# Optimization experiments

Measured on AMD Instinct MI355X. Metric: run time of the kernel, lower is better.

The kernel has to match this reference:

```python
import jax, jax.numpy as jnp
import numpy as np


def _maxpool2x2(x):
    # x: [B, C, H, W] -> [B, C, H//2, W//2]
    B, C, H, W = x.shape
    return x.reshape(B, C, H // 2, 2, W // 2, 2).max(axis=(3, 5))


def setup_inputs() -> dict:
    key = jax.random.key(0)
    ks = jax.random.split(key, 6)
    B, CH, H, W = 16, 128, 64, 64
    W_SCALE = 0.05  # keep pre-softmax logits in a sane range
    x = jax.random.normal(ks[0], (B, CH, H, W), dtype=jnp.float32)
    w_theta = jax.random.normal(ks[1], (CH // 8, CH), dtype=jnp.float32) * W_SCALE
    w_phi = jax.random.normal(ks[2], (CH // 8, CH), dtype=jnp.float32) * W_SCALE
    w_g = jax.random.normal(ks[3], (CH // 2, CH), dtype=jnp.float32) * W_SCALE
    w_o = jax.random.normal(ks[4], (CH, CH // 2), dtype=jnp.float32) * W_SCALE
    gamma = jax.random.normal(ks[5], (1,), dtype=jnp.float32)  # torch inits to 0; randomized for non-trivial output
    return {"x": x, "w_theta": w_theta, "w_phi": w_phi, "w_g": w_g, "w_o": w_o, "gamma": gamma}


def reference(x, w_theta, w_phi, w_g, w_o, gamma):
    B, C, H, W = x.shape
    N = H * W
    # 1x1 convs are channel GEMMs
    theta = jnp.einsum('oc,bchw->bohw', w_theta, x)          # [B, C/8, H, W]
    phi = _maxpool2x2(jnp.einsum('oc,bchw->bohw', w_phi, x))  # [B, C/8, H/2, W/2]
    g = _maxpool2x2(jnp.einsum('oc,bchw->bohw', w_g, x))      # [B, C/2, H/2, W/2]
    theta = theta.reshape(B, C // 8, N)        # [B, C/8, N]
    phi = phi.reshape(B, C // 8, N // 4)       # [B, C/8, N/4]
    g = g.reshape(B, C // 2, N // 4)           # [B, C/2, N/4]
    scores = jnp.einsum('bcn,bcm->bnm', theta, phi)  # [B, N, N/4]
    beta = jax.nn.softmax(scores, axis=-1)
    o = jnp.einsum('bcm,bnm->bcn', g, beta)          # [B, C/2, N]
    o = o.reshape(B, C // 2, H, W)
    o = jnp.einsum('oc,bchw->bohw', w_o, o)          # [B, C, H, W]
    return gamma[0] * o + x
```

## Files before the change

### kernel.cpp

```cpp
#include <hip/hip_runtime.h>


typedef __attribute__((ext_vector_type(8))) short bf16x8;
typedef __attribute__((ext_vector_type(16))) float f32x16;

#define LOG2E 1.4426950408889634f

__device__ __forceinline__ ushort f2bf(float f) {
    uint u = __float_as_uint(f);
    u += 0x7FFFu + ((u >> 16) & 1u);
    return (ushort)(u >> 16);
}
__device__ __forceinline__ uint pk2(float a, float b) {
    return (uint)f2bf(a) | ((uint)f2bf(b) << 16);
}

__global__ __launch_bounds__(256) void k_convs(const float* __restrict__ x,
                                               const float* __restrict__ w_theta,
                                               const float* __restrict__ w_phi,
                                               const float* __restrict__ w_g,
                                               ushort* __restrict__ theta_b,
                                               ushort* __restrict__ phi_b,
                                               ushort* __restrict__ g_b) {
    const int tid = threadIdx.x;
    const bool gpart = blockIdx.x >= 256;
    const int pb = blockIdx.x & 255;
    const int gq = pb * 64 + (tid >> 2);
    const int sub = tid & 3;
    const int b = gq >> 10, m = gq & 1023;
    const int h2 = m >> 5, w2 = m & 31;
    const int n = (2 * h2 + (sub >> 1)) * 64 + 2 * w2 + (sub & 1);
    const float* xp = x + (size_t)b * 128 * 4096 + n;

    if (!gpart) {
        __shared__ float wt[128][32];
        for (int i = tid; i < 2048; i += 256) { int o = i >> 7, c = i & 127; wt[c][o] = w_theta[i] * LOG2E; }
        for (int i = tid; i < 2048; i += 256) { int o = i >> 7, c = i & 127; wt[c][16 + o] = w_phi[i]; }
        __syncthreads();
        float th[16], ph[16];
#pragma unroll
        for (int o = 0; o < 16; ++o) { th[o] = 0.f; ph[o] = 0.f; }
        for (int c = 0; c < 128; ++c) {
            float xv = xp[(size_t)c * 4096];
            const float* wr = wt[c];
#pragma unroll
            for (int o = 0; o < 16; ++o) th[o] = fmaf(wr[o], xv, th[o]);
#pragma unroll
            for (int o = 0; o < 16; ++o) ph[o] = fmaf(wr[16 + o], xv, ph[o]);
        }
        uint4 t0, t1;
        t0.x = pk2(th[0], th[1]);  t0.y = pk2(th[2], th[3]);
        t0.z = pk2(th[4], th[5]);  t0.w = pk2(th[6], th[7]);
        t1.x = pk2(th[8], th[9]);  t1.y = pk2(th[10], th[11]);
        t1.z = pk2(th[12], th[13]); t1.w = pk2(th[14], th[15]);
        uint4* tp = (uint4*)(theta_b + ((size_t)b * 4096 + n) * 16);
        tp[0] = t0; tp[1] = t1;
#pragma unroll
        for (int o = 0; o < 16; ++o) {
            ph[o] = fmaxf(ph[o], __shfl_xor(ph[o], 1));
            ph[o] = fmaxf(ph[o], __shfl_xor(ph[o], 2));
        }
        if (sub == 0) {
            uint4 p0, p1;
            p0.x = pk2(ph[0], ph[1]);  p0.y = pk2(ph[2], ph[3]);
            p0.z = pk2(ph[4], ph[5]);  p0.w = pk2(ph[6], ph[7]);
            p1.x = pk2(ph[8], ph[9]);  p1.y = pk2(ph[10], ph[11]);
            p1.z = pk2(ph[12], ph[13]); p1.w = pk2(ph[14], ph[15]);
            uint4* pp = (uint4*)(phi_b + ((size_t)b * 1024 + m) * 16);
            pp[0] = p0; pp[1] = p1;
        }
    } else {
        __shared__ float wg[128][64];
        __shared__ ushort gt[64][68];
        for (int i = tid; i < 8192; i += 256) { int o = i >> 7, c = i & 127; wg[c][o] = w_g[i]; }
        __syncthreads();
        float gg[64];
#pragma unroll
        for (int o = 0; o < 64; ++o) gg[o] = 0.f;
        for (int c = 0; c < 128; ++c) {
            float xv = xp[(size_t)c * 4096];
            const float* wr = wg[c];
#pragma unroll
            for (int o = 0; o < 64; ++o) gg[o] = fmaf(wr[o], xv, gg[o]);
        }
#pragma unroll
        for (int o = 0; o < 64; ++o) {
            gg[o] = fmaxf(gg[o], __shfl_xor(gg[o], 1));
            gg[o] = fmaxf(gg[o], __shfl_xor(gg[o], 2));
        }
        const int mq = tid >> 2;
        if (sub == 0) {
#pragma unroll
            for (int cc = 0; cc < 16; ++cc) gt[cc][mq] = f2bf(gg[cc]);
        } else if (sub == 1) {
#pragma unroll
            for (int cc = 0; cc < 16; ++cc) gt[16 + cc][mq] = f2bf(gg[16 + cc]);
        } else if (sub == 2) {
#pragma unroll
            for (int cc = 0; cc < 16; ++cc) gt[32 + cc][mq] = f2bf(gg[32 + cc]);
        } else {
#pragma unroll
            for (int cc = 0; cc < 16; ++cc) gt[48 + cc][mq] = f2bf(gg[48 + cc]);
        }
        __syncthreads();
        const int c = tid >> 2, q = tid & 3;
        const uint2* s = (const uint2*)&gt[c][16 * q];
        uint2 v0 = s[0], v1 = s[1], v2 = s[2], v3 = s[3];
        const int bb = pb >> 4, mb = (pb & 15) * 64;
        uint2* dst = (uint2*)(g_b + ((size_t)bb * 64 + c) * 1024 + mb + 16 * q);
        dst[0] = v0; dst[1] = v1; dst[2] = v2; dst[3] = v3;
    }
}

__global__ __launch_bounds__(256) void k_attn(const ushort* __restrict__ theta_b,
                                              const ushort* __restrict__ phi_b,
                                              const ushort* __restrict__ g_b,
                                              const float* __restrict__ w_o,
                                              const float* __restrict__ x,
                                              const float* __restrict__ gamma,
                                              float* __restrict__ out) {
    const int tid = threadIdx.x;
    const int wave = tid >> 6, lane = tid & 63;
    const int l31 = lane & 31, h = lane >> 5;
    const int b = blockIdx.x >> 5, nt = blockIdx.x & 31;
    const int n = nt * 128 + wave * 32 + l31;

    bf16x8 thf = *(const bf16x8*)(theta_b + ((size_t)b * 4096 + n) * 16 + h * 8);

    const ushort* pbase = phi_b + (size_t)b * 1024 * 16 + h * 8;
    const ushort* gbase = g_b + ((size_t)b * 64 + l31) * 1024 + 8 * h;

    f32x16 o0 = {0,0,0,0,0,0,0,0,0,0,0,0,0,0,0,0};
    f32x16 o1 = {0,0,0,0,0,0,0,0,0,0,0,0,0,0,0,0};
    float sm0 = 0.f, sm1 = 0.f;

    bf16x8 phf = *(const bf16x8*)(pbase + (size_t)l31 * 16);
    bf16x8 gA0 = *(const bf16x8*)(gbase);
    bf16x8 gA1 = *(const bf16x8*)(gbase + 32 * 1024);
    bf16x8 gB0 = *(const bf16x8*)(gbase + 16);
    bf16x8 gB1 = *(const bf16x8*)(gbase + 16 + 32 * 1024);

    for (int mt = 0; mt < 32; ++mt) {
        const int m1 = ((mt + 1) & 31) * 32;
        bf16x8 nphf = *(const bf16x8*)(pbase + (size_t)(m1 + l31) * 16);
        bf16x8 ngA0 = *(const bf16x8*)(gbase + m1);
        bf16x8 ngA1 = *(const bf16x8*)(gbase + m1 + 32 * 1024);
        bf16x8 ngB0 = *(const bf16x8*)(gbase + m1 + 16);
        bf16x8 ngB1 = *(const bf16x8*)(gbase + m1 + 16 + 32 * 1024);

        f32x16 S = {0,0,0,0,0,0,0,0,0,0,0,0,0,0,0,0};
        S = __builtin_amdgcn_mfma_f32_32x32x16_bf16(phf, thf, S, 0, 0, 0);
        float p[16];
#pragma unroll
        for (int jj = 0; jj < 16; ++jj) p[jj] = exp2f(S[jj]);
        sm0 += ((p[0] + p[1]) + (p[2] + p[3])) + ((p[4] + p[5]) + (p[6] + p[7]));
        sm1 += ((p[8] + p[9]) + (p[10] + p[11])) + ((p[12] + p[13]) + (p[14] + p[15]));

        uint c0 = pk2(p[0], p[1]),   c1 = pk2(p[2], p[3]);
        uint c2 = pk2(p[4], p[5]),   c3 = pk2(p[6], p[7]);
        uint c4 = pk2(p[8], p[9]),   c5 = pk2(p[10], p[11]);
        uint c6 = pk2(p[12], p[13]), c7 = pk2(p[14], p[15]);
        uint q0 = (uint)__shfl_xor((int)(h ? c0 : c2), 32);
        uint q1 = (uint)__shfl_xor((int)(h ? c1 : c3), 32);
        uint q2 = (uint)__shfl_xor((int)(h ? c4 : c6), 32);
        uint q3 = (uint)__shfl_xor((int)(h ? c5 : c7), 32);
        union { bf16x8 v; uint u[4]; } B0, B1;
        if (h == 0) {
            B0.u[0] = c0; B0.u[1] = c1; B0.u[2] = q0; B0.u[3] = q1;
            B1.u[0] = c4; B1.u[1] = c5; B1.u[2] = q2; B1.u[3] = q3;
        } else {
            B0.u[0] = q0; B0.u[1] = q1; B0.u[2] = c2; B0.u[3] = c3;
            B1.u[0] = q2; B1.u[1] = q3; B1.u[2] = c6; B1.u[3] = c7;
        }
        o0 = __builtin_amdgcn_mfma_f32_32x32x16_bf16(gA0, B0.v, o0, 0, 0, 0);
        o1 = __builtin_amdgcn_mfma_f32_32x32x16_bf16(gA1, B0.v, o1, 0, 0, 0);
        o0 = __builtin_amdgcn_mfma_f32_32x32x16_bf16(gB0, B1.v, o0, 0, 0, 0);
        o1 = __builtin_amdgcn_mfma_f32_32x32x16_bf16(gB1, B1.v, o1, 0, 0, 0);

        phf = nphf; gA0 = ngA0; gA1 = ngA1; gB0 = ngB0; gB1 = ngB1;
    }
    float sm = sm0 + sm1;
    sm += __shfl_xor(sm, 32);
    const float inv = 1.f / sm;
#pragma unroll
    for (int jj = 0; jj < 16; ++jj) { o0[jj] *= inv; o1[jj] *= inv; }

    bf16x8 Bf[4];
#pragma unroll
    for (int kc = 0; kc < 4; ++kc) {
        const f32x16& oo = (kc < 2) ? o0 : o1;
        const int base = 8 * (kc & 1);
        uint Pa0 = pk2(oo[base + 0], oo[base + 1]);
        uint Pa1 = pk2(oo[base + 2], oo[base + 3]);
        uint Pb0 = pk2(oo[base + 4], oo[base + 5]);
        uint Pb1 = pk2(oo[base + 6], oo[base + 7]);
        uint z0 = h ? Pa0 : Pb0, z1 = h ? Pa1 : Pb1;
        uint r0 = (uint)__shfl_xor((int)z0, 32);
        uint r1 = (uint)__shfl_xor((int)z1, 32);
        union { bf16x8 v; uint u[4]; } Bx;
        if (h == 0) { Bx.u[0] = Pa0; Bx.u[1] = Pa1; Bx.u[2] = r0;  Bx.u[3] = r1; }
        else        { Bx.u[0] = r0;  Bx.u[1] = r1;  Bx.u[2] = Pb0; Bx.u[3] = Pb1; }
        Bf[kc] = Bx.v;
    }

    const float gm = gamma[0];
#pragma unroll
    for (int cof = 0; cof < 4; ++cof) {
        f32x16 oc = {0,0,0,0,0,0,0,0,0,0,0,0,0,0,0,0};
#pragma unroll
        for (int kc = 0; kc < 4; ++kc) {
            const float* wp = w_o + (32 * cof + l31) * 64 + 16 * kc + 8 * h;
            float4 wa = *(const float4*)(wp);
            float4 wb = *(const float4*)(wp + 4);
            union { bf16x8 v; uint u[4]; } W;
            W.u[0] = pk2(wa.x, wa.y); W.u[1] = pk2(wa.z, wa.w);
            W.u[2] = pk2(wb.x, wb.y); W.u[3] = pk2(wb.z, wb.w);
            oc = __builtin_amdgcn_mfma_f32_32x32x16_bf16(W.v, Bf[kc], oc, 0, 0, 0);
        }
#pragma unroll
        for (int jj = 0; jj < 16; ++jj) {
            int co = 32 * cof + (jj & 3) + 8 * (jj >> 2) + 4 * h;
            size_t idx = ((size_t)(b * 128 + co)) * 4096 + n;
            out[idx] = fmaf(gm, oc[jj], x[idx]);
        }
    }
}

extern "C" void kernel_launch(void* const* d_in, const int* in_sizes, int n_in,
                              void* d_out, int out_size, void* d_ws, size_t ws_size,
                              hipStream_t stream) {
    const float* x       = (const float*)d_in[0];
    const float* w_theta = (const float*)d_in[1];
    const float* w_phi   = (const float*)d_in[2];
    const float* w_g     = (const float*)d_in[3];
    const float* w_o     = (const float*)d_in[4];
    const float* gamma   = (const float*)d_in[5];
    float* out = (float*)d_out;

    ushort* theta_b = (ushort*)d_ws;
    ushort* phi_b   = theta_b + 1048576;
    ushort* g_b     = phi_b + 262144;

    k_convs<<<512, 256, 0, stream>>>(x, w_theta, w_phi, w_g, theta_b, phi_b, g_b);
    k_attn<<<512, 256, 0, stream>>>(theta_b, phi_b, g_b, w_o, x, gamma, out);
}
```

Measured before the change: 167.9 us.

## Split g-conv across two blocks, use hardware exp2 and bf16 pack in attention

The g projection in the conv kernel is split into two halves handled by separate blocks (768 blocks instead of 512). Each thread now keeps 32 accumulators instead of 64, which lowers register pressure and raises parallelism, at the cost of reading x one more time. In the attention kernel, exp2f is replaced with the raw v_exp_f32 instruction and the manual bf16 rounding with the hardware float2-to-bf16x2 conversion, cutting ALU work in the softmax inner loop. The raw v_exp_f32 skips exp2f's denormal and range handling, which could change results slightly for extreme inputs.

```diff
diff --git a/kernel.cpp b/kernel.cpp
--- a/kernel.cpp
+++ b/kernel.cpp
@@ -1,4 +1,5 @@
 #include <hip/hip_runtime.h>
+#include <hip/hip_bf16.h>
 
 
 typedef __attribute__((ext_vector_type(8))) short bf16x8;
@@ -13,6 +14,16 @@
 }
 __device__ __forceinline__ uint pk2(float a, float b) {
     return (uint)f2bf(a) | ((uint)f2bf(b) << 16);
+}
+__device__ __forceinline__ uint pk2hw(float a, float b) {
+    union { __hip_bfloat162 h; uint u; } cv;
+    cv.h = __float22bfloat162_rn(make_float2(a, b));
+    return cv.u;
+}
+__device__ __forceinline__ float exp2_hw(float v) {
+    float r;
+    asm("v_exp_f32 %0, %1" : "=v"(r) : "v"(v));
+    return r;
 }
 
 __global__ __launch_bounds__(256) void k_convs(const float* __restrict__ x,
@@ -22,8 +33,9 @@
                                                ushort* __restrict__ theta_b,
                                                ushort* __restrict__ phi_b,
                                                ushort* __restrict__ g_b) {
+    __shared__ __align__(16) char smem[16384 + 32 * 72 * 2];
     const int tid = threadIdx.x;
-    const bool gpart = blockIdx.x >= 256;
+    const int part = blockIdx.x >> 8;
     const int pb = blockIdx.x & 255;
     const int gq = pb * 64 + (tid >> 2);
     const int sub = tid & 3;
@@ -32,8 +44,8 @@
     const int n = (2 * h2 + (sub >> 1)) * 64 + 2 * w2 + (sub & 1);
     const float* xp = x + (size_t)b * 128 * 4096 + n;
 
-    if (!gpart) {
-        __shared__ float wt[128][32];
+    if (part == 0) {
+        float (*wt)[32] = (float (*)[32])smem;
         for (int i = tid; i < 2048; i += 256) { int o = i >> 7, c = i & 127; wt[c][o] = w_theta[i] * LOG2E; }
         for (int i = tid; i < 2048; i += 256) { int o = i >> 7, c = i & 127; wt[c][16 + o] = w_phi[i]; }
         __syncthreads();
@@ -70,45 +82,33 @@
             pp[0] = p0; pp[1] = p1;
         }
     } else {
-        __shared__ float wg[128][64];
-        __shared__ ushort gt[64][68];
-        for (int i = tid; i < 8192; i += 256) { int o = i >> 7, c = i & 127; wg[c][o] = w_g[i]; }
+        const int gp = part - 1;
+        float (*wg)[32] = (float (*)[32])smem;
+        ushort (*gt)[72] = (ushort (*)[72])(smem + 16384);
+        for (int i = tid; i < 4096; i += 256) { int o = i >> 7, c = i & 127; wg[c][o] = w_g[(gp * 32 + o) * 128 + c]; }
         __syncthreads();
-        float gg[64];
-#pragma unroll
-        for (int o = 0; o < 64; ++o) gg[o] = 0.f;
+        float gg[32];
+#pragma unroll
+        for (int o = 0; o < 32; ++o) gg[o] = 0.f;
         for (int c = 0; c < 128; ++c) {
             float xv = xp[(size_t)c * 4096];
             const float* wr = wg[c];
 #pragma unroll
-            for (int o = 0; o < 64; ++o) gg[o] = fmaf(wr[o], xv, gg[o]);
-        }
-#pragma unroll
-        for (int o = 0; o < 64; ++o) {
+            for (int o = 0; o < 32; ++o) gg[o] = fmaf(wr[o], xv, gg[o]);
+        }
+#pragma unroll
+        for (int o = 0; o < 32; ++o) {
             gg[o] = fmaxf(gg[o], __shfl_xor(gg[o], 1));
             gg[o] = fmaxf(gg[o], __shfl_xor(gg[o], 2));
         }
-        const int mq = tid >> 2;
-        if (sub == 0) {
-#pragma unroll
-            for (int cc = 0; cc < 16; ++cc) gt[cc][mq] = f2bf(gg[cc]);
-        } else if (sub == 1) {
-#pragma unroll
-            for (int cc = 0; cc < 16; ++cc) gt[16 + cc][mq] = f2bf(gg[16 + cc]);
-        } else if (sub == 2) {
-#pragma unroll
-            for (int cc = 0; cc < 16; ++cc) gt[32 + cc][mq] = f2bf(gg[32 + cc]);
-        } else {
-#pragma unroll
-            for (int cc = 0; cc < 16; ++cc) gt[48 + cc][mq] = f2bf(gg[48 + cc]);
-        }
+        const int col = tid >> 2;
+#pragma unroll
+        for (int cc = 0; cc < 8; ++cc) gt[8 * sub + cc][col] = f2bf(gg[8 * sub + cc]);
         __syncthreads();
-        const int c = tid >> 2, q = tid & 3;
-        const uint2* s = (const uint2*)&gt[c][16 * q];
-        uint2 v0 = s[0], v1 = s[1], v2 = s[2], v3 = s[3];
+        const int cl = tid >> 3, q = tid & 7;
+        uint4 v = *(const uint4*)&gt[cl][8 * q];
         const int bb = pb >> 4, mb = (pb & 15) * 64;
-        uint2* dst = (uint2*)(g_b + ((size_t)bb * 64 + c) * 1024 + mb + 16 * q);
-        dst[0] = v0; dst[1] = v1; dst[2] = v2; dst[3] = v3;
+        *(uint4*)(g_b + ((size_t)bb * 64 + gp * 32 + cl) * 1024 + mb + 8 * q) = v;
     }
 }
 
@@ -152,14 +152,14 @@
         S = __builtin_amdgcn_mfma_f32_32x32x16_bf16(phf, thf, S, 0, 0, 0);
         float p[16];
 #pragma unroll
-        for (int jj = 0; jj < 16; ++jj) p[jj] = exp2f(S[jj]);
+        for (int jj = 0; jj < 16; ++jj) p[jj] = exp2_hw(S[jj]);
         sm0 += ((p[0] + p[1]) + (p[2] + p[3])) + ((p[4] + p[5]) + (p[6] + p[7]));
         sm1 += ((p[8] + p[9]) + (p[10] + p[11])) + ((p[12] + p[13]) + (p[14] + p[15]));
 
-        uint c0 = pk2(p[0], p[1]),   c1 = pk2(p[2], p[3]);
-        uint c2 = pk2(p[4], p[5]),   c3 = pk2(p[6], p[7]);
-        uint c4 = pk2(p[8], p[9]),   c5 = pk2(p[10], p[11]);
-        uint c6 = pk2(p[12], p[13]), c7 = pk2(p[14], p[15]);
+        uint c0 = pk2hw(p[0], p[1]),   c1 = pk2hw(p[2], p[3]);
+        uint c2 = pk2hw(p[4], p[5]),   c3 = pk2hw(p[6], p[7]);
+        uint c4 = pk2hw(p[8], p[9]),   c5 = pk2hw(p[10], p[11]);
+        uint c6 = pk2hw(p[12], p[13]), c7 = pk2hw(p[14], p[15]);
         uint q0 = (uint)__shfl_xor((int)(h ? c0 : c2), 32);
         uint q1 = (uint)__shfl_xor((int)(h ? c1 : c3), 32);
         uint q2 = (uint)__shfl_xor((int)(h ? c4 : c6), 32);
@@ -241,6 +241,6 @@
     ushort* phi_b   = theta_b + 1048576;
     ushort* g_b     = phi_b + 262144;
 
-    k_convs<<<512, 256, 0, stream>>>(x, w_theta, w_phi, w_g, theta_b, phi_b, g_b);
+    k_convs<<<768, 256, 0, stream>>>(x, w_theta, w_phi, w_g, theta_b, phi_b, g_b);
     k_attn<<<512, 256, 0, stream>>>(theta_b, phi_b, g_b, w_o, x, gamma, out);
 }
```

Result: faster. 162.5 us (-3.3%).
